# Optimization experiments

Measured on AMD Instinct MI355X. Metric: run time of the kernel, lower is better.

Reference implementation:

```python
import jax, jax.numpy as jnp
import numpy as np

B, N, D, S, H = 64, 4096, 256, 8, 256
ITERS = 3
EPS = 1e-8
SCALE = D ** -0.5


def _ln(x, g, b):
    m = jnp.mean(x, axis=-1, keepdims=True)
    v = jnp.mean((x - m) ** 2, axis=-1, keepdims=True)
    return (x - m) * jax.lax.rsqrt(v + 1e-5) * g + b


def setup_inputs() -> dict:
    key = jax.random.key(0)
    ks = jax.random.split(key, 12)
    s = 0.02
    return {
        'inputs': jax.random.normal(ks[0], (B, N, D), jnp.float32),
        'slot_noise': jax.random.normal(ks[1], (B, S, D), jnp.float32),
        'slots_mean': jax.random.normal(ks[2], (1, 1, D), jnp.float32),
        'slots_logvar': s * jax.random.normal(ks[3], (1, 1, D), jnp.float32),
        'Wq': s * jax.random.normal(ks[4], (D, D), jnp.float32),
        'bq': jnp.zeros((D,), jnp.float32),
        'Wk': s * jax.random.normal(ks[5], (D, D), jnp.float32),
        'bk': jnp.zeros((D,), jnp.float32),
        'Wv': s * jax.random.normal(ks[6], (D, D), jnp.float32),
        'bv': jnp.zeros((D,), jnp.float32),
        'W_ih': s * jax.random.normal(ks[7], (3 * D, D), jnp.float32),
        'b_ih': jnp.zeros((3 * D,), jnp.float32),
        'W_hh': s * jax.random.normal(ks[8], (3 * D, D), jnp.float32),
        'b_hh': jnp.zeros((3 * D,), jnp.float32),
        'W1': s * jax.random.normal(ks[9], (H, D), jnp.float32),
        'b1': jnp.zeros((H,), jnp.float32),
        'W2': s * jax.random.normal(ks[10], (D, H), jnp.float32),
        'b2': jnp.zeros((D,), jnp.float32),
        'g_in': jnp.ones((D,), jnp.float32),
        'bias_in': jnp.zeros((D,), jnp.float32),
        'g_slots': jnp.ones((D,), jnp.float32),
        'bias_slots': jnp.zeros((D,), jnp.float32),
        'g_ff': jnp.ones((D,), jnp.float32),
        'bias_ff': jnp.zeros((D,), jnp.float32),
    }


def reference(inputs, slot_noise, slots_mean, slots_logvar, Wq, bq, Wk, bk, Wv, bv,
              W_ih, b_ih, W_hh, b_hh, W1, b1, W2, b2,
              g_in, bias_in, g_slots, bias_slots, g_ff, bias_ff):
    # slot init: mean + exp(logvar) * noise  (exp(logvar) used as multiplier, as in source)
    slots = slots_mean + jnp.exp(slots_logvar) * slot_noise  # [B,S,D]
    x = _ln(inputs, g_in, bias_in)                            # [B,N,D]
    k = x @ Wk.T + bk
    v = x @ Wv.T + bv
    attn = None
    for _ in range(ITERS):
        slots_prev = slots
        sn = _ln(slots, g_slots, bias_slots)
        q = sn @ Wq.T + bq                                    # [B,S,D]
        dots = jnp.einsum('bid,bjd->bij', q, k) * SCALE       # [B,S,N]
        attn = jax.nn.softmax(dots, axis=1) + EPS             # softmax over slots, no renorm
        updates = jnp.einsum('bjd,bij->bid', v, attn)         # [B,S,D]
        # GRUCell (PyTorch convention)
        gi = updates @ W_ih.T + b_ih                          # [B,S,3D]
        gh = slots_prev @ W_hh.T + b_hh
        i_r, i_z, i_n = jnp.split(gi, 3, axis=-1)
        h_r, h_z, h_n = jnp.split(gh, 3, axis=-1)
        r = jax.nn.sigmoid(i_r + h_r)
        z = jax.nn.sigmoid(i_z + h_z)
        n = jnp.tanh(i_n + r * h_n)
        slots = (1.0 - z) * n + z * slots_prev
        # MLP residual
        sf = _ln(slots, g_ff, bias_ff)
        slots = slots + (jax.nn.relu(sf @ W1.T + b1) @ W2.T + b2)
    return (slots, attn)
```

## Files before the change

kernel.cpp:

```cpp
#include <hip/hip_runtime.h>

typedef unsigned short u16;
typedef __bf16 bf16x8 __attribute__((ext_vector_type(8)));
typedef float f32x4 __attribute__((ext_vector_type(4)));

#define DEV static __device__ __forceinline__

DEV u16 f2bf(float f) {
    unsigned int u = __builtin_bit_cast(unsigned int, f);
    u += 0x7FFFu + ((u >> 16) & 1u);
    return (u16)(u >> 16);
}

DEV bf16x8 frag_ld(const u16* p) {
    return __builtin_bit_cast(bf16x8, *(const uint4*)p);
}

DEV float sigm(float x) { return 1.f / (1.f + __expf(-x)); }

DEV float blo(unsigned u) { return __builtin_bit_cast(float, u << 16); }
DEV float bhi(unsigned u) { return __builtin_bit_cast(float, u & 0xffff0000u); }

__global__ __launch_bounds__(256) void kSetup(
    const float* __restrict__ noise, const float* __restrict__ mean,
    const float* __restrict__ logv, float* __restrict__ slots,
    const float* __restrict__ Wq, const float* __restrict__ Wk,
    const float* __restrict__ bq, const float* __restrict__ bk,
    float* __restrict__ Wqk, float* __restrict__ wbc,
    const float* __restrict__ Wv,  float* __restrict__ WvT,
    const float* __restrict__ Wih, float* __restrict__ WihT,
    const float* __restrict__ Whh, float* __restrict__ WhhT,
    const float* __restrict__ W1,  float* __restrict__ W1T,
    const float* __restrict__ W2,  float* __restrict__ W2T)
{
    __shared__ float tile[32][33];
    const int bid = blockIdx.x, t = threadIdx.x;
    if (bid < 512) {
        const int id = bid * 256 + t;
        const int d = id & 255;
        slots[id] = mean[d] + __expf(logv[d]) * noise[id];
        return;
    }
    if (bid < 770) {
        const int a = bid - 512, e = t;
        if (a < 256) {
            float acc = 0.f;
            for (int d = 0; d < 256; ++d) acc += Wq[(size_t)d * 256 + a] * Wk[(size_t)d * 256 + e];
            Wqk[(size_t)a * 256 + e] = acc;
        } else if (a == 256) {
            float acc = 0.f;
            for (int d = 0; d < 256; ++d) acc += bq[d] * Wk[(size_t)d * 256 + e];
            wbc[e] = acc;
        } else {
            float acc = 0.f;
            for (int d = 0; d < 256; ++d) acc += Wq[(size_t)d * 256 + e] * bk[d];
            wbc[256 + e] = acc;
            if (e == 0) {
                float c0 = 0.f;
                for (int d = 0; d < 256; ++d) c0 += bq[d] * bk[d];
                wbc[512] = c0;
            }
        }
        return;
    }
    const int rb = bid - 770;
    const float* in; float* outp; int R, k;
    if (rb < 64)       { in = Wv;  outp = WvT;  R = 256; k = rb; }
    else if (rb < 256) { in = Wih; outp = WihT; R = 768; k = rb - 64; }
    else if (rb < 448) { in = Whh; outp = WhhT; R = 768; k = rb - 256; }
    else if (rb < 512) { in = W1;  outp = W1T;  R = 256; k = rb - 448; }
    else               { in = W2;  outp = W2T;  R = 256; k = rb - 512; }
    const int bx = k & 7, by = k >> 3;
    const int tx = t & 31, ty = t >> 5;
    const int c0 = bx * 32, r0 = by * 32;
    #pragma unroll
    for (int i = 0; i < 4; ++i)
        tile[ty + i * 8][tx] = in[(size_t)(r0 + ty + i * 8) * 256 + c0 + tx];
    __syncthreads();
    #pragma unroll
    for (int i = 0; i < 4; ++i)
        outp[(size_t)(c0 + ty + i * 8) * R + r0 + tx] = tile[tx][ty + i * 8];
}

__global__ __launch_bounds__(256) void kSn(
    const float* __restrict__ slots, const float* __restrict__ gs, const float* __restrict__ bs,
    const float* __restrict__ Wqk, const float* __restrict__ wbc,
    u16* __restrict__ qo, float* __restrict__ qc)
{
    __shared__ float SN[8][256];
    __shared__ float red2[4][8][64];
    const int t = threadIdx.x;
    const int b = blockIdx.y, seg = blockIdx.x;
    const int w = t >> 6, lane = t & 63;
    #pragma unroll
    for (int rr = 0; rr < 2; ++rr) {
        const int r = w * 2 + rr;
        const int c = lane * 4;
        const float4 x = *(const float4*)(slots + ((size_t)b * 8 + r) * 256 + c);
        float s1 = x.x + x.y + x.z + x.w;
        float s2 = x.x * x.x + x.y * x.y + x.z * x.z + x.w * x.w;
        #pragma unroll
        for (int o = 32; o > 0; o >>= 1) { s1 += __shfl_xor(s1, o); s2 += __shfl_xor(s2, o); }
        const float mu = s1 * (1.f / 256.f);
        const float rs = rsqrtf(s2 * (1.f / 256.f) - mu * mu + 1e-5f);
        const float4 g4 = *(const float4*)(gs + c);
        const float4 b4 = *(const float4*)(bs + c);
        SN[r][c + 0] = (x.x - mu) * rs * g4.x + b4.x;
        SN[r][c + 1] = (x.y - mu) * rs * g4.y + b4.y;
        SN[r][c + 2] = (x.z - mu) * rs * g4.z + b4.z;
        SN[r][c + 3] = (x.w - mu) * rs * g4.w + b4.w;
    }
    __syncthreads();
    const int c = seg * 64 + (t & 63);
    const int p = t >> 6;
    float acc[8] = {};
    #pragma unroll 4
    for (int d = p * 64; d < p * 64 + 64; ++d) {
        const float wq = Wqk[(size_t)d * 256 + c];
        #pragma unroll
        for (int r = 0; r < 8; ++r) acc[r] += wq * SN[r][d];
    }
    #pragma unroll
    for (int r = 0; r < 8; ++r) red2[p][r][t & 63] = acc[r];
    __syncthreads();
    const float bb = wbc[c];
    #pragma unroll
    for (int rr = t >> 6; rr < 8; rr += 4) {
        const float s = red2[0][rr][t & 63] + red2[1][rr][t & 63]
                      + red2[2][rr][t & 63] + red2[3][rr][t & 63];
        qo[((size_t)b * 16 + rr) * 256 + c] = f2bf((s + bb) * 0.0625f);
    }
    if (seg == 0) {
        const int r = t >> 5, l = t & 31;
        float a = 0.f;
        #pragma unroll
        for (int d8 = 0; d8 < 8; ++d8) a += SN[r][l * 8 + d8] * wbc[256 + l * 8 + d8];
        #pragma unroll
        for (int o = 16; o > 0; o >>= 1) a += __shfl_xor(a, o);
        if (l == 0) qc[(size_t)b * 8 + r] = 0.0625f * (a + wbc[512]);
    }
}

template<int FUSE>
__global__ __launch_bounds__(256, 2) void kF(
    const float* __restrict__ X,
    const float* __restrict__ gin, const float* __restrict__ bin,
    const u16* __restrict__ Q,
    const float* __restrict__ qcg,
    u16* __restrict__ XN,
    float* __restrict__ attn_out,
    float* __restrict__ part,
    float* __restrict__ part2,
    int write_attn)
{
    __shared__ __align__(16) float att32[128][8];
    __shared__ float usred[4][8][256];
    __shared__ float sred[4][2][4][16];
    const int tid = threadIdx.x;
    const int w = tid >> 6, lane = tid & 63;
    const int quad = lane >> 4, l16 = lane & 15;
    const int dsg = lane & 31, jg = lane >> 5;
    const int b = blockIdx.y, nt = blockIdx.x;
    const int j0 = nt << 8;
    const size_t rowbase = (size_t)b * 4096 + j0;

    const u16* qb = Q + (size_t)b * 16 * 256;
    bf16x8 qfrag[8];
    #pragma unroll
    for (int k0 = 0; k0 < 8; ++k0)
        qfrag[k0] = frag_ld(qb + l16 * 256 + k0 * 32 + quad * 8);

    float c8[8];
    #pragma unroll
    for (int i = 0; i < 8; ++i) c8[i] = qcg[(size_t)b * 8 + i];

    float4 g4, b4;
    if (FUSE) {
        const int cc = lane << 2;
        g4 = *(const float4*)(gin + cc);
        b4 = *(const float4*)(bin + cc);
    }

    float acc[8][8];
    #pragma unroll
    for (int i = 0; i < 8; ++i)
        #pragma unroll
        for (int e = 0; e < 8; ++e) acc[i][e] = 0.f;
    float sacc[4] = {};

    const u16* xb = XN + rowbase * 256;
    const int qb1 = (quad & 1) << 2;

    for (int st = 0; st < 2; ++st) {
        if (FUSE) {
            const int cc = lane << 2;
            #pragma unroll 4
            for (int i = 0; i < 32; ++i) {
                const size_t gr = rowbase + st * 128 + w * 32 + i;
                const float4 x = *(const float4*)(X + gr * 256 + cc);
                float s1 = x.x + x.y + x.z + x.w;
                float s2 = x.x * x.x + x.y * x.y + x.z * x.z + x.w * x.w;
                #pragma unroll
                for (int o = 32; o > 0; o >>= 1) { s1 += __shfl_xor(s1, o); s2 += __shfl_xor(s2, o); }
                const float mu = s1 * (1.f / 256.f);
                const float rs = rsqrtf(s2 * (1.f / 256.f) - mu * mu + 1e-5f);
                ushort4 pk;
                pk.x = f2bf((x.x - mu) * rs * g4.x + b4.x);
                pk.y = f2bf((x.y - mu) * rs * g4.y + b4.y);
                pk.z = f2bf((x.z - mu) * rs * g4.z + b4.z);
                pk.w = f2bf((x.w - mu) * rs * g4.w + b4.w);
                *(ushort4*)(XN + gr * 256 + cc) = pk;
            }
            asm volatile("s_waitcnt vmcnt(0)" ::: "memory");
        }
        f32x4 dacc[2] = {};
        #pragma unroll
        for (int n2 = 0; n2 < 2; ++n2) {
            const int jsl = w * 32 + n2 * 16 + l16;
            const u16* xrow = xb + ((size_t)(st * 128 + jsl)) * 256;
            #pragma unroll
            for (int k0 = 0; k0 < 8; ++k0) {
                const bf16x8 bfr = frag_ld(xrow + k0 * 32 + quad * 8);
                dacc[n2] = __builtin_amdgcn_mfma_f32_16x16x32_bf16(
                    qfrag[k0], bfr, dacc[n2], 0, 0, 0);
            }
        }
        #pragma unroll
        for (int n2 = 0; n2 < 2; ++n2) {
            const int jsl = w * 32 + n2 * 16 + l16;
            float v[8];
            #pragma unroll
            for (int r = 0; r < 4; ++r) {
                v[qb1 + r]       = dacc[n2][r];
                v[(qb1 ^ 4) + r] = __shfl_xor(dacc[n2][r], 16);
            }
            #pragma unroll
            for (int i = 0; i < 8; ++i) v[i] += c8[i];
            float m = v[0];
            #pragma unroll
            for (int i = 1; i < 8; ++i) m = fmaxf(m, v[i]);
            float s = 0.f;
            #pragma unroll
            for (int i = 0; i < 8; ++i) { v[i] = __expf(v[i] - m); s += v[i]; }
            const float inv = 1.f / s;
            if (quad < 2) {
                float4 av;
                av.x = v[qb1 + 0] * inv + 1e-8f;
                av.y = v[qb1 + 1] * inv + 1e-8f;
                av.z = v[qb1 + 2] * inv + 1e-8f;
                av.w = v[qb1 + 3] * inv + 1e-8f;
                sacc[0] += av.x; sacc[1] += av.y; sacc[2] += av.z; sacc[3] += av.w;
                *(float4*)&att32[jsl][qb1] = av;
                if (write_attn) {
                    attn_out[((size_t)b * 8 + qb1 + 0) * 4096 + j0 + st * 128 + jsl] = av.x;
                    attn_out[((size_t)b * 8 + qb1 + 1) * 4096 + j0 + st * 128 + jsl] = av.y;
                    attn_out[((size_t)b * 8 + qb1 + 2) * 4096 + j0 + st * 128 + jsl] = av.z;
                    attn_out[((size_t)b * 8 + qb1 + 3) * 4096 + j0 + st * 128 + jsl] = av.w;
                }
            }
        }
        #pragma unroll 4
        for (int jj = 0; jj < 16; ++jj) {
            const int jsl = w * 32 + jj * 2 + jg;
            const uint4 raw = *(const uint4*)(xb + ((size_t)(st * 128 + jsl)) * 256 + dsg * 8);
            const float4 a0 = *(const float4*)&att32[jsl][0];
            const float4 a1 = *(const float4*)&att32[jsl][4];
            float xf[8];
            xf[0] = blo(raw.x); xf[1] = bhi(raw.x);
            xf[2] = blo(raw.y); xf[3] = bhi(raw.y);
            xf[4] = blo(raw.z); xf[5] = bhi(raw.z);
            xf[6] = blo(raw.w); xf[7] = bhi(raw.w);
            #pragma unroll
            for (int e = 0; e < 8; ++e) {
                acc[0][e] = fmaf(a0.x, xf[e], acc[0][e]);
                acc[1][e] = fmaf(a0.y, xf[e], acc[1][e]);
                acc[2][e] = fmaf(a0.z, xf[e], acc[2][e]);
                acc[3][e] = fmaf(a0.w, xf[e], acc[3][e]);
                acc[4][e] = fmaf(a1.x, xf[e], acc[4][e]);
                acc[5][e] = fmaf(a1.y, xf[e], acc[5][e]);
                acc[6][e] = fmaf(a1.z, xf[e], acc[6][e]);
                acc[7][e] = fmaf(a1.w, xf[e], acc[7][e]);
            }
        }
    }

    #pragma unroll
    for (int i = 0; i < 8; ++i)
        #pragma unroll
        for (int e = 0; e < 8; ++e) acc[i][e] += __shfl_xor(acc[i][e], 32);
    if (jg == 0) {
        #pragma unroll
        for (int i = 0; i < 8; ++i) {
            float4 lo, hi;
            lo.x = acc[i][0]; lo.y = acc[i][1]; lo.z = acc[i][2]; lo.w = acc[i][3];
            hi.x = acc[i][4]; hi.y = acc[i][5]; hi.z = acc[i][6]; hi.w = acc[i][7];
            *(float4*)&usred[w][i][dsg * 8]     = lo;
            *(float4*)&usred[w][i][dsg * 8 + 4] = hi;
        }
    }
    if (quad < 2) {
        #pragma unroll
        for (int r = 0; r < 4; ++r) sred[w][quad][r][l16] = sacc[r];
    }
    __syncthreads();
    #pragma unroll
    for (int i = 0; i < 8; ++i) {
        const float s = usred[0][i][tid] + usred[1][i][tid]
                      + usred[2][i][tid] + usred[3][i][tid];
        part[(((size_t)nt * 64 + b) * 8 + i) * 256 + tid] = s;
    }
    if (tid < 8) {
        const int q = tid >> 2, r = tid & 3;
        float s = 0.f;
        #pragma unroll
        for (int ww = 0; ww < 4; ++ww)
            #pragma unroll
            for (int l = 0; l < 16; ++l) s += sred[ww][q][r][l];
        part2[((size_t)nt * 64 + b) * 8 + tid] = s;
    }
}

__global__ __launch_bounds__(256) void kB3(
    const float* __restrict__ part, const float* __restrict__ part2,
    const float* __restrict__ WvT, const float* __restrict__ bv,
    const float* __restrict__ sl_in,
    const float* __restrict__ WihT, const float* __restrict__ bih,
    const float* __restrict__ WhhT, const float* __restrict__ bhh,
    const float* __restrict__ W1T, const float* __restrict__ b1,
    const float* __restrict__ W2T, const float* __restrict__ b2,
    const float* __restrict__ gf, const float* __restrict__ bff,
    float* __restrict__ sl_out)
{
    __shared__ float Ul[2][256], Sl[2][256];
    __shared__ float red[2][4][6][256];
    __shared__ float SNl[2][256];
    __shared__ float cw[2][2][4];
    __shared__ float Ssl[2];
    const int t = threadIdx.x;
    const int kp = t >> 6, c = t & 63;
    const int row0 = blockIdx.x * 2;

    #pragma unroll
    for (int r = 0; r < 2; ++r) {
        const int row = row0 + r;
        const int b = row >> 3, s = row & 7;
        float u = 0.f;
        #pragma unroll
        for (int nt = 0; nt < 16; ++nt)
            u += part[(((size_t)nt * 64 + b) * 8 + s) * 256 + t];
        Ul[r][t] = u;
        Sl[r][t] = sl_in[(size_t)row * 256 + t];
    }
    if (t < 2) {
        const int row = row0 + t;
        const int b = row >> 3, s = row & 7;
        float ss = 0.f;
        #pragma unroll
        for (int nt = 0; nt < 16; ++nt) ss += part2[((size_t)nt * 64 + b) * 8 + s];
        Ssl[t] = ss;
    }
    __syncthreads();

    {
        float va[2][4] = {};
        #pragma unroll 4
        for (int dd = 0; dd < 64; ++dd) {
            const int d = kp * 64 + dd;
            const float* wr = WvT + (size_t)d * 256;
            const float u0 = Ul[0][d], u1 = Ul[1][d];
            #pragma unroll
            for (int cg = 0; cg < 4; ++cg) {
                const float wv = wr[cg * 64 + c];
                va[0][cg] += wv * u0;
                va[1][cg] += wv * u1;
            }
        }
        #pragma unroll
        for (int r = 0; r < 2; ++r)
            #pragma unroll
            for (int cg = 0; cg < 4; ++cg)
                red[r][kp][0][cg * 64 + c] = va[r][cg];
    }
    __syncthreads();
    const float bvt = bv[t];
    float upd2[2];
    #pragma unroll
    for (int r = 0; r < 2; ++r)
        upd2[r] = red[r][0][0][t] + red[r][1][0][t] + red[r][2][0][t] + red[r][3][0][t]
                + Ssl[r] * bvt;
    __syncthreads();
    #pragma unroll
    for (int r = 0; r < 2; ++r) Ul[r][t] = upd2[r];
    __syncthreads();

    float ga[2][4][6] = {};
    #pragma unroll 2
    for (int dd = 0; dd < 64; ++dd) {
        const int d = kp * 64 + dd;
        const float* wi = WihT + (size_t)d * 768;
        const float* wh = WhhT + (size_t)d * 768;
        const float u0 = Ul[0][d], u1 = Ul[1][d];
        const float s0 = Sl[0][d], s1 = Sl[1][d];
        #pragma unroll
        for (int cg = 0; cg < 4; ++cg) {
            const int t2 = cg * 64 + c;
            const float wa = wi[t2], wb = wi[256 + t2], wc = wi[512 + t2];
            const float wd = wh[t2], we = wh[256 + t2], wf = wh[512 + t2];
            ga[0][cg][0] += wa * u0; ga[0][cg][1] += wb * u0; ga[0][cg][2] += wc * u0;
            ga[0][cg][3] += wd * s0; ga[0][cg][4] += we * s0; ga[0][cg][5] += wf * s0;
            ga[1][cg][0] += wa * u1; ga[1][cg][1] += wb * u1; ga[1][cg][2] += wc * u1;
            ga[1][cg][3] += wd * s1; ga[1][cg][4] += we * s1; ga[1][cg][5] += wf * s1;
        }
    }
    #pragma unroll
    for (int r = 0; r < 2; ++r)
        #pragma unroll
        for (int cg = 0; cg < 4; ++cg)
            #pragma unroll
            for (int g = 0; g < 6; ++g)
                red[r][kp][g][cg * 64 + c] = ga[r][cg][g];
    __syncthreads();

    const float b_ir = bih[t], b_iz = bih[256 + t], b_in = bih[512 + t];
    const float b_hr = bhh[t], b_hz = bhh[256 + t], b_hn = bhh[512 + t];
    float hnew[2];
    #pragma unroll
    for (int r = 0; r < 2; ++r) {
        float s6[6];
        #pragma unroll
        for (int g = 0; g < 6; ++g)
            s6[g] = red[r][0][g][t] + red[r][1][g][t] + red[r][2][g][t] + red[r][3][g][t];
        const float rg = sigm(s6[0] + b_ir + s6[3] + b_hr);
        const float zg = sigm(s6[1] + b_iz + s6[4] + b_hz);
        const float ng = tanhf(s6[2] + b_in + rg * (s6[5] + b_hn));
        hnew[r] = (1.f - zg) * ng + zg * Sl[r][t];
    }
    #pragma unroll
    for (int r = 0; r < 2; ++r) {
        float s1 = hnew[r], s2 = hnew[r] * hnew[r];
        #pragma unroll
        for (int o = 32; o > 0; o >>= 1) { s1 += __shfl_xor(s1, o); s2 += __shfl_xor(s2, o); }
        if (c == 0) { cw[r][0][kp] = s1; cw[r][1][kp] = s2; }
    }
    __syncthreads();
    const float gft = gf[t], bfft = bff[t];
    #pragma unroll
    for (int r = 0; r < 2; ++r) {
        const float s1 = cw[r][0][0] + cw[r][0][1] + cw[r][0][2] + cw[r][0][3];
        const float s2 = cw[r][1][0] + cw[r][1][1] + cw[r][1][2] + cw[r][1][3];
        const float mu = s1 * (1.f / 256.f);
        const float rs = rsqrtf(s2 * (1.f / 256.f) - mu * mu + 1e-5f);
        SNl[r][t] = (hnew[r] - mu) * rs * gft + bfft;
    }
    __syncthreads();

    {
        float m1[2][4] = {};
        #pragma unroll 4
        for (int dd = 0; dd < 64; ++dd) {
            const int d = kp * 64 + dd;
            const float* wr = W1T + (size_t)d * 256;
            const float n0 = SNl[0][d], n1 = SNl[1][d];
            #pragma unroll
            for (int cg = 0; cg < 4; ++cg) {
                const float wv = wr[cg * 64 + c];
                m1[0][cg] += wv * n0;
                m1[1][cg] += wv * n1;
            }
        }
        #pragma unroll
        for (int r = 0; r < 2; ++r)
            #pragma unroll
            for (int cg = 0; cg < 4; ++cg)
                red[r][kp][0][cg * 64 + c] = m1[r][cg];
    }
    __syncthreads();
    const float b1t = b1[t];
    float h1v[2];
    #pragma unroll
    for (int r = 0; r < 2; ++r)
        h1v[r] = fmaxf(red[r][0][0][t] + red[r][1][0][t] + red[r][2][0][t] + red[r][3][0][t]
                       + b1t, 0.f);
    __syncthreads();
    #pragma unroll
    for (int r = 0; r < 2; ++r) SNl[r][t] = h1v[r];
    __syncthreads();
    {
        float m2[2][4] = {};
        #pragma unroll 4
        for (int dd = 0; dd < 64; ++dd) {
            const int d = kp * 64 + dd;
            const float* wr = W2T + (size_t)d * 256;
            const float x0 = SNl[0][d], x1 = SNl[1][d];
            #pragma unroll
            for (int cg = 0; cg < 4; ++cg) {
                const float wv = wr[cg * 64 + c];
                m2[0][cg] += wv * x0;
                m2[1][cg] += wv * x1;
            }
        }
        #pragma unroll
        for (int r = 0; r < 2; ++r)
            #pragma unroll
            for (int cg = 0; cg < 4; ++cg)
                red[r][kp][1][cg * 64 + c] = m2[r][cg];
    }
    __syncthreads();
    const float b2t = b2[t];
    #pragma unroll
    for (int r = 0; r < 2; ++r) {
        const float o = red[r][0][1][t] + red[r][1][1][t] + red[r][2][1][t] + red[r][3][1][t];
        sl_out[(size_t)(row0 + r) * 256 + t] = hnew[r] + o + b2t;
    }
}

extern "C" void kernel_launch(void* const* d_in, const int* in_sizes, int n_in,
                              void* d_out, int out_size, void* d_ws, size_t ws_size,
                              hipStream_t stream) {
    const float* inputs = (const float*)d_in[0];
    const float* noise  = (const float*)d_in[1];
    const float* smean  = (const float*)d_in[2];
    const float* slogv  = (const float*)d_in[3];
    const float* Wq  = (const float*)d_in[4];
    const float* bq  = (const float*)d_in[5];
    const float* Wk  = (const float*)d_in[6];
    const float* bk  = (const float*)d_in[7];
    const float* Wv  = (const float*)d_in[8];
    const float* bv  = (const float*)d_in[9];
    const float* Wih = (const float*)d_in[10];
    const float* bih = (const float*)d_in[11];
    const float* Whh = (const float*)d_in[12];
    const float* bhh = (const float*)d_in[13];
    const float* W1  = (const float*)d_in[14];
    const float* b1  = (const float*)d_in[15];
    const float* W2  = (const float*)d_in[16];
    const float* b2  = (const float*)d_in[17];
    const float* gin = (const float*)d_in[18];
    const float* bin = (const float*)d_in[19];
    const float* gs  = (const float*)d_in[20];
    const float* bs  = (const float*)d_in[21];
    const float* gf  = (const float*)d_in[22];
    const float* bff = (const float*)d_in[23];

    char* ws = (char*)d_ws;
    u16*  XNw    = (u16*)(ws);
    u16*  qw     = (u16*)(ws + 134217728ull);
    float* slots = (float*)(ws + 134742016ull);
    float* Wqkw  = (float*)(ws + 135266304ull);
    float* wbc   = (float*)(ws + 135528448ull);
    float* qcw   = (float*)(ws + 135532544ull);
    float* WvT   = (float*)(ws + 135536640ull);
    float* WihT  = (float*)(ws + 135798784ull);
    float* WhhT  = (float*)(ws + 136585216ull);
    float* W1T   = (float*)(ws + 137371648ull);
    float* W2T   = (float*)(ws + 137633792ull);
    float* partw = (float*)(ws + 137895936ull);
    float* part2w= (float*)(ws + 146284544ull);

    float* out = (float*)d_out;
    float* attn_out = out + 131072;

    kSetup<<<1346, 256, 0, stream>>>(noise, smean, slogv, slots,
                                     Wq, Wk, bq, bk, Wqkw, wbc,
                                     Wv, WvT, Wih, WihT, Whh, WhhT, W1, W1T, W2, W2T);
    for (int it = 0; it < 3; ++it) {
        kSn<<<dim3(4, 64), 256, 0, stream>>>(slots, gs, bs, Wqkw, wbc, qw, qcw);
        if (it == 0)
            kF<1><<<dim3(16, 64), 256, 0, stream>>>(inputs, gin, bin, qw, qcw, XNw,
                                                    attn_out, partw, part2w, 0);
        else
            kF<0><<<dim3(16, 64), 256, 0, stream>>>(inputs, gin, bin, qw, qcw, XNw,
                                                    attn_out, partw, part2w, it == 2);
        kB3<<<256, 256, 0, stream>>>(partw, part2w, WvT, bv, slots,
                                     WihT, bih, WhhT, bhh, W1T, b1, W2T, b2, gf, bff,
                                     (it == 2) ? out : slots);
    }
}
```

Measured before the change: 715.6 us.

## Stage XN tile in swizzled LDS, drop block reduction, write per-wave partials

kF now copies each 64-row chunk of normalized inputs into a swizzled LDS stash. The MFMA dot-product pass and the attention-weighted update pass both read it, so the second global read of XN goes away, and the first iteration feeds the MFMA directly from the fused layernorm output. The cross-wave LDS reduction and its __syncthreads are removed. Each wave writes its own partial sums, which quadruples the partial buffer that kB3 must sum (64 units instead of 16). It also uses packed f32x2 FMAs for the update accumulation and raises launch bounds to 3 blocks per SM, which may increase register pressure.

Result: slower. 888.9 us (+24.2%).

```diff
diff --git a/kernel.cpp b/kernel.cpp
--- a/kernel.cpp
+++ b/kernel.cpp
@@ -3,6 +3,7 @@
 typedef unsigned short u16;
 typedef __bf16 bf16x8 __attribute__((ext_vector_type(8)));
 typedef float f32x4 __attribute__((ext_vector_type(4)));
+typedef float f32x2 __attribute__((ext_vector_type(2)));
 
 #define DEV static __device__ __forceinline__
 
@@ -20,6 +21,9 @@
 
 DEV float blo(unsigned u) { return __builtin_bit_cast(float, u << 16); }
 DEV float bhi(unsigned u) { return __builtin_bit_cast(float, u & 0xffff0000u); }
+DEV f32x2 bf2(unsigned u) { return (f32x2){ blo(u), bhi(u) }; }
+
+DEV int sw(int row, int colu16) { return row * 256 + (colu16 ^ ((row & 7) << 3)); }
 
 __global__ __launch_bounds__(256) void kSetup(
     const float* __restrict__ noise, const float* __restrict__ mean,
@@ -142,7 +146,7 @@
 }
 
 template<int FUSE>
-__global__ __launch_bounds__(256, 2) void kF(
+__global__ __launch_bounds__(256, 3) void kF(
     const float* __restrict__ X,
     const float* __restrict__ gin, const float* __restrict__ bin,
     const u16* __restrict__ Q,
@@ -153,22 +157,22 @@
     float* __restrict__ part2,
     int write_attn)
 {
-    __shared__ __align__(16) float att32[128][8];
-    __shared__ float usred[4][8][256];
-    __shared__ float sred[4][2][4][16];
+    __shared__ __align__(16) u16 stash[64 * 256];
+    __shared__ __align__(16) float att32[64][8];
     const int tid = threadIdx.x;
     const int w = tid >> 6, lane = tid & 63;
     const int quad = lane >> 4, l16 = lane & 15;
     const int dsg = lane & 31, jg = lane >> 5;
+    const int qb1 = (quad & 1) << 2;
     const int b = blockIdx.y, nt = blockIdx.x;
     const int j0 = nt << 8;
     const size_t rowbase = (size_t)b * 4096 + j0;
 
-    const u16* qb = Q + (size_t)b * 16 * 256;
+    const u16* qptr = Q + (size_t)b * 16 * 256;
     bf16x8 qfrag[8];
     #pragma unroll
     for (int k0 = 0; k0 < 8; ++k0)
-        qfrag[k0] = frag_ld(qb + l16 * 256 + k0 * 32 + quad * 8);
+        qfrag[k0] = frag_ld(qptr + l16 * 256 + k0 * 32 + quad * 8);
 
     float c8[8];
     #pragma unroll
@@ -181,22 +185,20 @@
         b4 = *(const float4*)(bin + cc);
     }
 
-    float acc[8][8];
+    f32x2 acc2[8][4];
     #pragma unroll
     for (int i = 0; i < 8; ++i)
         #pragma unroll
-        for (int e = 0; e < 8; ++e) acc[i][e] = 0.f;
+        for (int k = 0; k < 4; ++k) acc2[i][k] = (f32x2){0.f, 0.f};
     float sacc[4] = {};
 
-    const u16* xb = XN + rowbase * 256;
-    const int qb1 = (quad & 1) << 2;
-
-    for (int st = 0; st < 2; ++st) {
+    for (int st = 0; st < 4; ++st) {
+        const int srow = w * 16;
         if (FUSE) {
             const int cc = lane << 2;
             #pragma unroll 4
-            for (int i = 0; i < 32; ++i) {
-                const size_t gr = rowbase + st * 128 + w * 32 + i;
+            for (int i = 0; i < 16; ++i) {
+                const size_t gr = rowbase + st * 64 + srow + i;
                 const float4 x = *(const float4*)(X + gr * 256 + cc);
                 float s1 = x.x + x.y + x.z + x.w;
                 float s2 = x.x * x.x + x.y * x.y + x.z * x.z + x.w * x.w;
@@ -210,29 +212,32 @@
                 pk.z = f2bf((x.z - mu) * rs * g4.z + b4.z);
                 pk.w = f2bf((x.w - mu) * rs * g4.w + b4.w);
                 *(ushort4*)(XN + gr * 256 + cc) = pk;
-            }
-            asm volatile("s_waitcnt vmcnt(0)" ::: "memory");
-        }
-        f32x4 dacc[2] = {};
-        #pragma unroll
-        for (int n2 = 0; n2 < 2; ++n2) {
-            const int jsl = w * 32 + n2 * 16 + l16;
-            const u16* xrow = xb + ((size_t)(st * 128 + jsl)) * 256;
+                *(ushort4*)(stash + sw(srow + i, cc)) = pk;
+            }
+        }
+        f32x4 dacc = {};
+        if (FUSE) {
             #pragma unroll
             for (int k0 = 0; k0 < 8; ++k0) {
-                const bf16x8 bfr = frag_ld(xrow + k0 * 32 + quad * 8);
-                dacc[n2] = __builtin_amdgcn_mfma_f32_16x16x32_bf16(
-                    qfrag[k0], bfr, dacc[n2], 0, 0, 0);
-            }
-        }
-        #pragma unroll
-        for (int n2 = 0; n2 < 2; ++n2) {
-            const int jsl = w * 32 + n2 * 16 + l16;
+                const bf16x8 bfr = frag_ld(stash + sw(srow + l16, k0 * 32 + quad * 8));
+                dacc = __builtin_amdgcn_mfma_f32_16x16x32_bf16(qfrag[k0], bfr, dacc, 0, 0, 0);
+            }
+        } else {
+            const u16* xrow = XN + (rowbase + st * 64 + srow + l16) * 256;
+            #pragma unroll
+            for (int k0 = 0; k0 < 8; ++k0) {
+                const uint4 raw = *(const uint4*)(xrow + k0 * 32 + quad * 8);
+                *(uint4*)(stash + sw(srow + l16, k0 * 32 + quad * 8)) = raw;
+                dacc = __builtin_amdgcn_mfma_f32_16x16x32_bf16(
+                    qfrag[k0], __builtin_bit_cast(bf16x8, raw), dacc, 0, 0, 0);
+            }
+        }
+        {
             float v[8];
             #pragma unroll
             for (int r = 0; r < 4; ++r) {
-                v[qb1 + r]       = dacc[n2][r];
-                v[(qb1 ^ 4) + r] = __shfl_xor(dacc[n2][r], 16);
+                v[qb1 + r]       = dacc[r];
+                v[(qb1 ^ 4) + r] = __shfl_xor(dacc[r], 16);
             }
             #pragma unroll
             for (int i = 0; i < 8; ++i) v[i] += c8[i];
@@ -250,36 +255,31 @@
                 av.z = v[qb1 + 2] * inv + 1e-8f;
                 av.w = v[qb1 + 3] * inv + 1e-8f;
                 sacc[0] += av.x; sacc[1] += av.y; sacc[2] += av.z; sacc[3] += av.w;
-                *(float4*)&att32[jsl][qb1] = av;
+                *(float4*)&att32[srow + l16][qb1] = av;
                 if (write_attn) {
-                    attn_out[((size_t)b * 8 + qb1 + 0) * 4096 + j0 + st * 128 + jsl] = av.x;
-                    attn_out[((size_t)b * 8 + qb1 + 1) * 4096 + j0 + st * 128 + jsl] = av.y;
-                    attn_out[((size_t)b * 8 + qb1 + 2) * 4096 + j0 + st * 128 + jsl] = av.z;
-                    attn_out[((size_t)b * 8 + qb1 + 3) * 4096 + j0 + st * 128 + jsl] = av.w;
+                    const size_t jglob = j0 + st * 64 + srow + l16;
+                    attn_out[((size_t)b * 8 + qb1 + 0) * 4096 + jglob] = av.x;
+                    attn_out[((size_t)b * 8 + qb1 + 1) * 4096 + jglob] = av.y;
+                    attn_out[((size_t)b * 8 + qb1 + 2) * 4096 + jglob] = av.z;
+                    attn_out[((size_t)b * 8 + qb1 + 3) * 4096 + jglob] = av.w;
                 }
             }
         }
-        #pragma unroll 4
-        for (int jj = 0; jj < 16; ++jj) {
-            const int jsl = w * 32 + jj * 2 + jg;
-            const uint4 raw = *(const uint4*)(xb + ((size_t)(st * 128 + jsl)) * 256 + dsg * 8);
-            const float4 a0 = *(const float4*)&att32[jsl][0];
-            const float4 a1 = *(const float4*)&att32[jsl][4];
-            float xf[8];
-            xf[0] = blo(raw.x); xf[1] = bhi(raw.x);
-            xf[2] = blo(raw.y); xf[3] = bhi(raw.y);
-            xf[4] = blo(raw.z); xf[5] = bhi(raw.z);
-            xf[6] = blo(raw.w); xf[7] = bhi(raw.w);
-            #pragma unroll
-            for (int e = 0; e < 8; ++e) {
-                acc[0][e] = fmaf(a0.x, xf[e], acc[0][e]);
-                acc[1][e] = fmaf(a0.y, xf[e], acc[1][e]);
-                acc[2][e] = fmaf(a0.z, xf[e], acc[2][e]);
-                acc[3][e] = fmaf(a0.w, xf[e], acc[3][e]);
-                acc[4][e] = fmaf(a1.x, xf[e], acc[4][e]);
-                acc[5][e] = fmaf(a1.y, xf[e], acc[5][e]);
-                acc[6][e] = fmaf(a1.z, xf[e], acc[6][e]);
-                acc[7][e] = fmaf(a1.w, xf[e], acc[7][e]);
+        #pragma unroll
+        for (int jj = 0; jj < 8; ++jj) {
+            const int row = srow + jj * 2 + jg;
+            const uint4 raw = *(const uint4*)(stash + sw(row, dsg * 8));
+            const float4 a0 = *(const float4*)&att32[row][0];
+            const float4 a1 = *(const float4*)&att32[row][4];
+            f32x2 xf[4];
+            xf[0] = bf2(raw.x); xf[1] = bf2(raw.y); xf[2] = bf2(raw.z); xf[3] = bf2(raw.w);
+            const float av8[8] = {a0.x, a0.y, a0.z, a0.w, a1.x, a1.y, a1.z, a1.w};
+            #pragma unroll
+            for (int i = 0; i < 8; ++i) {
+                const f32x2 aa = (f32x2){av8[i], av8[i]};
+                #pragma unroll
+                for (int k = 0; k < 4; ++k)
+                    acc2[i][k] = aa * xf[k] + acc2[i][k];
             }
         }
     }
@@ -287,36 +287,30 @@
     #pragma unroll
     for (int i = 0; i < 8; ++i)
         #pragma unroll
-        for (int e = 0; e < 8; ++e) acc[i][e] += __shfl_xor(acc[i][e], 32);
+        for (int k = 0; k < 4; ++k) {
+            acc2[i][k][0] += __shfl_xor(acc2[i][k][0], 32);
+            acc2[i][k][1] += __shfl_xor(acc2[i][k][1], 32);
+        }
+    const int unit = nt * 4 + w;
     if (jg == 0) {
+        const size_t pb = ((size_t)unit * 64 + b) * 8;
         #pragma unroll
         for (int i = 0; i < 8; ++i) {
             float4 lo, hi;
-            lo.x = acc[i][0]; lo.y = acc[i][1]; lo.z = acc[i][2]; lo.w = acc[i][3];
-            hi.x = acc[i][4]; hi.y = acc[i][5]; hi.z = acc[i][6]; hi.w = acc[i][7];
-            *(float4*)&usred[w][i][dsg * 8]     = lo;
-            *(float4*)&usred[w][i][dsg * 8 + 4] = hi;
-        }
-    }
-    if (quad < 2) {
-        #pragma unroll
-        for (int r = 0; r < 4; ++r) sred[w][quad][r][l16] = sacc[r];
-    }
-    __syncthreads();
-    #pragma unroll
-    for (int i = 0; i < 8; ++i) {
-        const float s = usred[0][i][tid] + usred[1][i][tid]
-                      + usred[2][i][tid] + usred[3][i][tid];
-        part[(((size_t)nt * 64 + b) * 8 + i) * 256 + tid] = s;
-    }
-    if (tid < 8) {
-        const int q = tid >> 2, r = tid & 3;
-        float s = 0.f;
-        #pragma unroll
-        for (int ww = 0; ww < 4; ++ww)
-            #pragma unroll
-            for (int l = 0; l < 16; ++l) s += sred[ww][q][r][l];
-        part2[((size_t)nt * 64 + b) * 8 + tid] = s;
+            lo.x = acc2[i][0][0]; lo.y = acc2[i][0][1]; lo.z = acc2[i][1][0]; lo.w = acc2[i][1][1];
+            hi.x = acc2[i][2][0]; hi.y = acc2[i][2][1]; hi.z = acc2[i][3][0]; hi.w = acc2[i][3][1];
+            *(float4*)&part[(pb + i) * 256 + dsg * 8]     = lo;
+            *(float4*)&part[(pb + i) * 256 + dsg * 8 + 4] = hi;
+        }
+    }
+    #pragma unroll
+    for (int r = 0; r < 4; ++r)
+        #pragma unroll
+        for (int o = 1; o < 16; o <<= 1) sacc[r] += __shfl_xor(sacc[r], o);
+    if (l16 == 0 && quad < 2) {
+        #pragma unroll
+        for (int r = 0; r < 4; ++r)
+            part2[((size_t)unit * 64 + b) * 8 + qb1 + r] = sacc[r];
     }
 }
 
@@ -344,11 +338,13 @@
     for (int r = 0; r < 2; ++r) {
         const int row = row0 + r;
         const int b = row >> 3, s = row & 7;
-        float u = 0.f;
-        #pragma unroll
-        for (int nt = 0; nt < 16; ++nt)
-            u += part[(((size_t)nt * 64 + b) * 8 + s) * 256 + t];
-        Ul[r][t] = u;
+        float ua0 = 0.f, ua1 = 0.f;
+        #pragma unroll 8
+        for (int u = 0; u < 64; u += 2) {
+            ua0 += part[(((size_t)u * 64 + b) * 8 + s) * 256 + t];
+            ua1 += part[(((size_t)(u + 1) * 64 + b) * 8 + s) * 256 + t];
+        }
+        Ul[r][t] = ua0 + ua1;
         Sl[r][t] = sl_in[(size_t)row * 256 + t];
     }
     if (t < 2) {
@@ -356,7 +352,7 @@
         const int b = row >> 3, s = row & 7;
         float ss = 0.f;
         #pragma unroll
-        for (int nt = 0; nt < 16; ++nt) ss += part2[((size_t)nt * 64 + b) * 8 + s];
+        for (int u = 0; u < 64; ++u) ss += part2[((size_t)u * 64 + b) * 8 + s];
         Ssl[t] = ss;
     }
     __syncthreads();
@@ -555,7 +551,7 @@
     float* W1T   = (float*)(ws + 137371648ull);
     float* W2T   = (float*)(ws + 137633792ull);
     float* partw = (float*)(ws + 137895936ull);
-    float* part2w= (float*)(ws + 146284544ull);
+    float* part2w= (float*)(ws + 171450368ull);
 
     float* out = (float*)d_out;
     float* attn_out = out + 131072;
```
